# Kernel optimization log

Hardware: AMD Instinct MI355X
Metric: run time of the kernel (lower is better)

Reference implementation:

```python
import jax, jax.numpy as jnp
import numpy as np

N_NODES = 100000
N_EDGES = 3200000
NFEAT = 512
HDIM = 64
NCLASS = 40
N_LAYERS = 4
NEG_SLOPE = 0.2


def setup_inputs() -> dict:
    key = jax.random.key(0)
    ks = jax.random.split(key, 10)
    x = jax.random.normal(ks[0], (N_NODES, NFEAT), dtype=jnp.float32)
    edge_index = jax.random.randint(ks[1], (2, N_EDGES), 0, N_NODES, dtype=jnp.int64)
    s = 0.1
    return {
        "x": x,
        "edge_index": edge_index,
        "W_in": jax.random.normal(ks[2], (NFEAT, HDIM), dtype=jnp.float32) * s,
        "b_in": jnp.zeros((HDIM,), dtype=jnp.float32),
        "W_conv": jax.random.normal(ks[3], (N_LAYERS, HDIM, HDIM), dtype=jnp.float32) * s,
        "att_src": jax.random.normal(ks[4], (N_LAYERS, HDIM), dtype=jnp.float32) * s,
        "att_dst": jax.random.normal(ks[5], (N_LAYERS, HDIM), dtype=jnp.float32) * s,
        "b_conv": jnp.zeros((N_LAYERS, HDIM), dtype=jnp.float32),
        "W_out": jax.random.normal(ks[6], (HDIM, NCLASS), dtype=jnp.float32) * s,
        "b_out": jnp.zeros((NCLASS,), dtype=jnp.float32),
    }


def _gat_conv(x, src, dst, W, a_src_w, a_dst_w, bias):
    # PyG GATConv, heads=1, concat=True, add_self_loops handled by caller.
    N = x.shape[0]
    h = x @ W  # [N, H]
    a_src = h @ a_src_w  # [N]
    a_dst = h @ a_dst_w  # [N]
    e = jax.nn.leaky_relu(a_src[src] + a_dst[dst], NEG_SLOPE)  # [E]
    # segment softmax over edges grouped by destination node
    m = jax.ops.segment_max(e, dst, num_segments=N)
    ex = jnp.exp(e - m[dst])
    denom = jax.ops.segment_sum(ex, dst, num_segments=N)
    alpha = ex / denom[dst]
    out = jax.ops.segment_sum(alpha[:, None] * h[src], dst, num_segments=N)
    return out + bias


def reference(x, edge_index, W_in, b_in, W_conv, att_src, att_dst, b_conv, W_out, b_out):
    N = x.shape[0]
    # add self-loops (PyG GATConv default)
    loop = jnp.arange(N, dtype=edge_index.dtype)
    src = jnp.concatenate([edge_index[0], loop])
    dst = jnp.concatenate([edge_index[1], loop])

    h = x @ W_in + b_in  # lnin
    for l in range(N_LAYERS):
        h_in = h
        h = jax.nn.elu(_gat_conv(h, src, dst, W_conv[l], att_src[l], att_dst[l], b_conv[l]))
        h = h_in + h  # residual
    return h @ W_out + b_out  # lnout
```

## Files before the change

kernel.cpp:

```cpp
#include <hip/hip_runtime.h>
#include <hip/hip_bf16.h>
#include <hip/hip_fp16.h>

#define N_NODES 100000
#define N_EDGES 3200000
#define NFEAT 512
#define HDIM 64
#define NCLASS 40
#define N_LAYERS 4
#define NEG_SLOPE 0.2f

#define BATCH 4096
#define PBLOCKS ((N_EDGES + BATCH - 1) / BATCH)
#define SCUR_PAD 16

#define NB2 ((N_NODES + 255) / 256)
#define CAP2 9216
#define NCOUNT (NB2 * SCUR_PAD)

typedef __attribute__((ext_vector_type(8))) _Float16 half8;
typedef __attribute__((ext_vector_type(4))) float floatx4;

__device__ __forceinline__ float leaky(float x) {
    return x >= 0.f ? x : NEG_SLOPE * x;
}

__global__ void zero_counters_kernel(int* __restrict__ p) {
    int i = blockIdx.x * blockDim.x + threadIdx.x;
    if (i < NCOUNT) p[i] = 0;
}


__global__ __launch_bounds__(256) void partition_direct_kernel(const int* __restrict__ ei,
                                                               int* __restrict__ scur2,
                                                               unsigned* __restrict__ pairs2) {
    __shared__ unsigned buf[BATCH];
    __shared__ int cnt[NB2];
    __shared__ int off[NB2 + 1];
    __shared__ int gb[NB2];
    int t = threadIdx.x;
    long long base = (long long)blockIdx.x * BATCH;

    unsigned key[16];
    int bn[16];
    for (int i = t; i < NB2; i += 256) cnt[i] = 0;
    __syncthreads();

#pragma unroll
    for (int i = 0; i < 16; ++i) {
        long long e = base + i * 256 + t;
        if (e < N_EDGES) {
            int s = ei[e];
            int d = ei[N_EDGES + e];
            int b = d >> 8;
            bn[i] = b;
            key[i] = (unsigned)s | ((unsigned)(d & 255) << 17);
            atomicAdd(&cnt[b], 1);
        } else {
            bn[i] = -1;
        }
    }
    __syncthreads();
    if (t == 0) {
        int run = 0;
        for (int s2 = 0; s2 < NB2; ++s2) { off[s2] = run; run += cnt[s2]; }
        off[NB2] = run;
    }
    __syncthreads();
    for (int i = t; i < NB2; i += 256) {
        int c = cnt[i];
        gb[i] = c ? atomicAdd(&scur2[i * SCUR_PAD], c) : 0;
        cnt[i] = 0;
    }
    __syncthreads();
#pragma unroll
    for (int i = 0; i < 16; ++i) {
        if (bn[i] >= 0) {
            int p = atomicAdd(&cnt[bn[i]], 1);
            buf[off[bn[i]] + p] = key[i];
        }
    }
    __syncthreads();
    int total = off[NB2];
    for (int p = t; p < total; p += 256) {
        int lo = 0, hi = NB2 - 1;
        while (lo < hi) {
            int mid = (lo + hi + 1) >> 1;
            if (off[mid] <= p) lo = mid; else hi = mid - 1;
        }
        int idx = gb[lo] + (p - off[lo]);
        if (idx < CAP2) pairs2[(size_t)lo * CAP2 + idx] = buf[p];
    }
}

__global__ __launch_bounds__(512) void scan_buckets_kernel(const int* __restrict__ scur2,
                                                           int* __restrict__ bbase) {
    __shared__ int s[512];
    int t = threadIdx.x;
    int v = 0;
    if (t < NB2) {
        v = scur2[t * SCUR_PAD];
        if (v > CAP2) v = CAP2;
    }
    s[t] = v;
    __syncthreads();
    for (int off = 1; off < 512; off <<= 1) {
        int x = (t >= off) ? s[t - off] : 0;
        __syncthreads();
        s[t] += x;
        __syncthreads();
    }
    if (t < NB2) bbase[t] = s[t] - v;
    if (t == NB2 - 1) bbase[NB2] = s[t];
}

__global__ __launch_bounds__(256) void bucket_sort_kernel(const int* __restrict__ scur2,
                                                          const int* __restrict__ bbase,
                                                          const unsigned* __restrict__ pairs2,
                                                          int* __restrict__ col,
                                                          int* __restrict__ rp) {
    __shared__ int hist[256];
    __shared__ int cur[256];
    __shared__ unsigned outb[CAP2];
    int b = blockIdx.x;
    int c = scur2[b * SCUR_PAD]; if (c > CAP2) c = CAP2;
    const unsigned* seg = pairs2 + (size_t)b * CAP2;
    int t = threadIdx.x;
    int nlo = b * 256;
    int nnodes = N_NODES - nlo; if (nnodes > 256) nnodes = 256;
    hist[t] = 0;
    __syncthreads();
    for (int i = t; i < c; i += 256) atomicAdd(&hist[(seg[i] >> 17) & 255], 1);
    __syncthreads();
    int v = hist[t];
    for (int off = 1; off < 256; off <<= 1) {
        int x = (t >= off) ? hist[t - off] : 0;
        __syncthreads();
        hist[t] += x;
        __syncthreads();
    }
    int excl = hist[t] - v;
    cur[t] = excl;
    int base = bbase[b];
    if (t < nnodes) rp[nlo + t] = base + excl;
    if (b == NB2 - 1 && t == 0) rp[N_NODES] = base + c;
    __syncthreads();
    for (int i = t; i < c; i += 256) {
        unsigned k = seg[i];
        int p = atomicAdd(&cur[(k >> 17) & 255], 1);
        outb[p] = k & 0x1FFFFu;
    }
    __syncthreads();
    for (int i = t; i < c; i += 256) col[base + i] = (int)outb[i];
}


__global__ __launch_bounds__(256) void gemm_in_mfma(const float* __restrict__ A,
                                                    const float* __restrict__ B,
                                                    const float* __restrict__ bias,
                                                    float* __restrict__ C, int M) {
    __shared__ _Float16 As[2][64][40];
    __shared__ _Float16 Bt[2][64][40];
    int t = threadIdx.x;
    int lane = t & 63;
    int wid = t >> 6;
    int row0 = blockIdx.x * 64;

    floatx4 acc[4];
#pragma unroll
    for (int ct = 0; ct < 4; ++ct) acc[ct] = (floatx4){0.f, 0.f, 0.f, 0.f};

#define STAGE_A(buf, kt)                                                           \
    {                                                                              \
        int r = t >> 2, kq = (t & 3) << 3;                                         \
        int gr = row0 + r;                                                         \
        float4 v0 = make_float4(0.f, 0.f, 0.f, 0.f), v1 = v0;                      \
        if (gr < M) {                                                              \
            v0 = *(const float4*)&A[(size_t)gr * 512 + (kt) * 32 + kq];            \
            v1 = *(const float4*)&A[(size_t)gr * 512 + (kt) * 32 + kq + 4];        \
        }                                                                          \
        half8 h;                                                                   \
        h[0] = (_Float16)v0.x; h[1] = (_Float16)v0.y;                              \
        h[2] = (_Float16)v0.z; h[3] = (_Float16)v0.w;                              \
        h[4] = (_Float16)v1.x; h[5] = (_Float16)v1.y;                              \
        h[6] = (_Float16)v1.z; h[7] = (_Float16)v1.w;                              \
        *(half8*)&As[buf][r][kq] = h;                                              \
    }

#define STAGE_B(buf, kt)                                                           \
    {                                                                              \
        int k = t >> 3, n0 = (t & 7) << 3;                                         \
        float4 w0 = *(const float4*)&B[(size_t)((kt) * 32 + k) * 64 + n0];         \
        float4 w1 = *(const float4*)&B[(size_t)((kt) * 32 + k) * 64 + n0 + 4];     \
        Bt[buf][n0 + 0][k] = (_Float16)w0.x; Bt[buf][n0 + 1][k] = (_Float16)w0.y;  \
        Bt[buf][n0 + 2][k] = (_Float16)w0.z; Bt[buf][n0 + 3][k] = (_Float16)w0.w;  \
        Bt[buf][n0 + 4][k] = (_Float16)w1.x; Bt[buf][n0 + 5][k] = (_Float16)w1.y;  \
        Bt[buf][n0 + 6][k] = (_Float16)w1.z; Bt[buf][n0 + 7][k] = (_Float16)w1.w;  \
    }

    STAGE_A(0, 0)
    STAGE_B(0, 0)
    __syncthreads();
    for (int kt = 0; kt < 16; ++kt) {
        int buf = kt & 1;
        if (kt < 15) {
            STAGE_A(buf ^ 1, kt + 1)
            STAGE_B(buf ^ 1, kt + 1)
        }
        half8 a = *(half8*)&As[buf][wid * 16 + (lane & 15)][(lane >> 4) * 8];
#pragma unroll
        for (int ct = 0; ct < 4; ++ct) {
            half8 b = *(half8*)&Bt[buf][ct * 16 + (lane & 15)][(lane >> 4) * 8];
            acc[ct] = __builtin_amdgcn_mfma_f32_16x16x32_f16(a, b, acc[ct], 0, 0, 0);
        }
        __syncthreads();
    }
#pragma unroll
    for (int ct = 0; ct < 4; ++ct) {
        int colg = ct * 16 + (lane & 15);
        float bv = bias[colg];
#pragma unroll
        for (int i = 0; i < 4; ++i) {
            int gr = row0 + wid * 16 + (lane >> 4) * 4 + i;
            if (gr < M) C[(size_t)gr * 64 + colg] = acc[ct][i] + bv;
        }
    }
#undef STAGE_A
#undef STAGE_B
}


__global__ __launch_bounds__(256) void gemm_fused_mfma(const float* __restrict__ A,
                                                       const float* __restrict__ W,
                                                       const float* __restrict__ att_s_g,
                                                       const float* __restrict__ att_d_g,
                                                       float* __restrict__ as_,
                                                       float* __restrict__ ad_,
                                                       __half* __restrict__ h2h, int M) {
    __shared__ _Float16 As[64][72];
    __shared__ _Float16 Wt[64][72];
    __shared__ float sATT[128];
    int t = threadIdx.x;
    int lane = t & 63;
    int wid = t >> 6;
    int row0 = blockIdx.x * 64;
    if (t < 128) sATT[t] = (t < 64) ? att_s_g[t] : att_d_g[t - 64];

    {
        int r = t >> 2, kq = (t & 3) << 4;
        int gr = row0 + r;
        float4 v0 = make_float4(0.f, 0.f, 0.f, 0.f), v1 = v0, v2 = v0, v3 = v0;
        if (gr < M) {
            const float* ap = &A[(size_t)gr * 64 + kq];
            v0 = *(const float4*)(ap + 0);
            v1 = *(const float4*)(ap + 4);
            v2 = *(const float4*)(ap + 8);
            v3 = *(const float4*)(ap + 12);
        }
        half8 h0, h1;
        h0[0] = (_Float16)v0.x; h0[1] = (_Float16)v0.y; h0[2] = (_Float16)v0.z; h0[3] = (_Float16)v0.w;
        h0[4] = (_Float16)v1.x; h0[5] = (_Float16)v1.y; h0[6] = (_Float16)v1.z; h0[7] = (_Float16)v1.w;
        h1[0] = (_Float16)v2.x; h1[1] = (_Float16)v2.y; h1[2] = (_Float16)v2.z; h1[3] = (_Float16)v2.w;
        h1[4] = (_Float16)v3.x; h1[5] = (_Float16)v3.y; h1[6] = (_Float16)v3.z; h1[7] = (_Float16)v3.w;
        *(half8*)&As[r][kq] = h0;
        *(half8*)&As[r][kq + 8] = h1;
    }
    {
        int k = t >> 2, n0 = (t & 3) << 4;
        const float* wp = &W[(size_t)k * 64 + n0];
        float4 w0 = *(const float4*)(wp + 0);
        float4 w1 = *(const float4*)(wp + 4);
        float4 w2 = *(const float4*)(wp + 8);
        float4 w3 = *(const float4*)(wp + 12);
        float wv[16] = {w0.x, w0.y, w0.z, w0.w, w1.x, w1.y, w1.z, w1.w,
                        w2.x, w2.y, w2.z, w2.w, w3.x, w3.y, w3.z, w3.w};
#pragma unroll
        for (int j = 0; j < 16; ++j) Wt[n0 + j][k] = (_Float16)wv[j];
    }
    __syncthreads();

    floatx4 acc[4];
#pragma unroll
    for (int ct = 0; ct < 4; ++ct) acc[ct] = (floatx4){0.f, 0.f, 0.f, 0.f};
#pragma unroll
    for (int kt = 0; kt < 2; ++kt) {
        half8 a = *(half8*)&As[wid * 16 + (lane & 15)][kt * 32 + (lane >> 4) * 8];
#pragma unroll
        for (int ct = 0; ct < 4; ++ct) {
            half8 b = *(half8*)&Wt[ct * 16 + (lane & 15)][kt * 32 + (lane >> 4) * 8];
            acc[ct] = __builtin_amdgcn_mfma_f32_16x16x32_f16(a, b, acc[ct], 0, 0, 0);
        }
    }

    int c15 = lane & 15;
    float ps[4] = {0.f, 0.f, 0.f, 0.f}, pd[4] = {0.f, 0.f, 0.f, 0.f};
#pragma unroll
    for (int ct = 0; ct < 4; ++ct) {
        float sa = sATT[ct * 16 + c15];
        float sd = sATT[64 + ct * 16 + c15];
#pragma unroll
        for (int i = 0; i < 4; ++i) {
            ps[i] += acc[ct][i] * sa;
            pd[i] += acc[ct][i] * sd;
        }
    }
#pragma unroll
    for (int off = 1; off < 16; off <<= 1) {
#pragma unroll
        for (int i = 0; i < 4; ++i) {
            ps[i] += __shfl_xor(ps[i], off);
            pd[i] += __shfl_xor(pd[i], off);
        }
    }
    if (c15 == 0) {
#pragma unroll
        for (int i = 0; i < 4; ++i) {
            int gr = row0 + wid * 16 + (lane >> 4) * 4 + i;
            if (gr < M) { as_[gr] = ps[i]; ad_[gr] = pd[i]; }
        }
    }
#pragma unroll
    for (int ct = 0; ct < 4; ++ct) {
        int colg = ct * 16 + c15;
#pragma unroll
        for (int i = 0; i < 4; ++i) {
            int gr = row0 + wid * 16 + (lane >> 4) * 4 + i;
            if (gr < M) h2h[(size_t)gr * 64 + colg] = __float2half(acc[ct][i]);
        }
    }
}


__global__ __launch_bounds__(256) void gat_aggregate(const int* __restrict__ rp,
                                                     const int* __restrict__ col,
                                                     const __half* __restrict__ h2h,
                                                     const float* __restrict__ as_,
                                                     const float* __restrict__ ad_,
                                                     const float* __restrict__ bias,
                                                     float* __restrict__ h ) {
    __shared__ int2 sw[4][64];
    int wv = threadIdx.x >> 6;
    int wid = blockIdx.x * 4 + wv;
    int lane = threadIdx.x & 63;
    if (wid >= N_NODES) return;
    int beg = rp[wid];
    int end = rp[wid + 1];
    float adv = ad_[wid];
    float m = leaky(as_[wid] + adv);

    float acc = __half2float(h2h[(size_t)wid * 64 + lane]);
    float wsum = 0.f;

    for (int j0 = beg; j0 < end; j0 += 64) {
        int rem = end - j0;
        int cnt = rem < 64 ? rem : 64;
        if (lane < cnt) {
            int s = col[j0 + lane];
            float w = __expf(leaky(as_[s] + adv) - m);
            wsum += w;
            sw[wv][lane] = make_int2(s, __float_as_int(w));
        }
        int j = 0;
        for (; j + 8 <= cnt; j += 8) {
            int2 p[8];
#pragma unroll
            for (int q = 0; q < 8; ++q) p[q] = sw[wv][j + q];
            __half hv[8];
#pragma unroll
            for (int q = 0; q < 8; ++q) hv[q] = h2h[(size_t)p[q].x * 64 + lane];
#pragma unroll
            for (int q = 0; q < 8; ++q)
                acc = fmaf(__int_as_float(p[q].y), __half2float(hv[q]), acc);
        }
        for (; j < cnt; ++j) {
            int2 p = sw[wv][j];
            acc = fmaf(__int_as_float(p.y),
                       __half2float(h2h[(size_t)p.x * 64 + lane]), acc);
        }
    }
#pragma unroll
    for (int off = 32; off; off >>= 1) wsum += __shfl_xor(wsum, off);
    float denom = wsum + 1.0f;

    float o = acc / denom + bias[lane];
    float e = (o > 0.f) ? o : expm1f(o);
    size_t idx = (size_t)wid * 64 + lane;
    h[idx] = h[idx] + e;
}


__global__ __launch_bounds__(256) void out_gemm(const float* __restrict__ h,
                                                const float* __restrict__ W,
                                                const float* __restrict__ b,
                                                float* __restrict__ out) {
    __shared__ float Ws[64 * 40];
    __shared__ float bs[40];
    int t = threadIdx.x;
    for (int idx = t; idx < 64 * 40; idx += 256) Ws[idx] = W[idx];
    if (t < 40) bs[t] = b[t];
    __syncthreads();
    int wid = blockIdx.x * (blockDim.x >> 6) + (t >> 6);
    int lane = t & 63;
    if (wid >= N_NODES) return;
    float hv = h[(size_t)wid * 64 + lane];
    float acc = (lane < 40) ? bs[lane] : 0.f;
#pragma unroll
    for (int k = 0; k < 64; ++k) {
        float hk = __shfl(hv, k);
        float wv = (lane < 40) ? Ws[k * 40 + lane] : 0.f;
        acc += hk * wv;
    }
    if (lane < 40) out[(size_t)wid * 40 + lane] = acc;
}


extern "C" void kernel_launch(void* const* d_in, const int* in_sizes, int n_in,
                              void* d_out, int out_size, void* d_ws, size_t ws_size,
                              hipStream_t stream) {
    const float* x        = (const float*)d_in[0];
    const int* ei         = (const int*)d_in[1];
    const float* W_in     = (const float*)d_in[2];
    const float* b_in     = (const float*)d_in[3];
    const float* W_conv   = (const float*)d_in[4];
    const float* att_src  = (const float*)d_in[5];
    const float* att_dst  = (const float*)d_in[6];
    const float* b_conv   = (const float*)d_in[7];
    const float* W_out    = (const float*)d_in[8];
    const float* b_out    = (const float*)d_in[9];
    float* out = (float*)d_out;

    char* w = (char*)d_ws;
    float*    hA    = (float*)w;    w += (size_t)N_NODES * 64 * 4;
    __half*   h2h   = (__half*)w;   w += (size_t)N_NODES * 64 * 2;
    float*    as_   = (float*)w;    w += (size_t)N_NODES * 4;
    float*    ad_   = (float*)w;    w += (size_t)N_NODES * 4;
    int*      rp    = (int*)w;      w += 400016;
    int*      scur2 = (int*)w;      w += NB2 * SCUR_PAD * 4;
    int*      bbase = (int*)w;      w += 4096;
    int*      col   = (int*)w;      w += (size_t)N_EDGES * 4;
    unsigned* pairs2= (unsigned*)w; w += (size_t)NB2 * CAP2 * 4;

    zero_counters_kernel<<<(NCOUNT + 255) / 256, 256, 0, stream>>>(scur2);
    partition_direct_kernel<<<PBLOCKS, 256, 0, stream>>>(ei, scur2, pairs2);
    scan_buckets_kernel<<<1, 512, 0, stream>>>(scur2, bbase);
    bucket_sort_kernel<<<NB2, 256, 0, stream>>>(scur2, bbase, pairs2, col, rp);

    gemm_in_mfma<<<(N_NODES + 63) / 64, 256, 0, stream>>>(x, W_in, b_in, hA, N_NODES);

    for (int l = 0; l < N_LAYERS; ++l) {
        gemm_fused_mfma<<<(N_NODES + 63) / 64, 256, 0, stream>>>(hA, W_conv + (size_t)l * 64 * 64,
                                                                 att_src + l * 64, att_dst + l * 64,
                                                                 as_, ad_, h2h, N_NODES);
        gat_aggregate<<<N_NODES / 4, 256, 0, stream>>>(rp, col, h2h, as_, ad_,
                                                       b_conv + l * 64, hA);
    }

    out_gemm<<<N_NODES / 4, 256, 0, stream>>>(hA, W_out, b_out, out);
}
```

Measured before the change: 611.9 us.

## Process two nodes per wavefront in aggregation and fuse output GEMM into last layer

The GAT aggregation kernel now handles two consecutive destination nodes per wavefront, packing both nodes' edge lists into shared 64-edge chunks and routing each contribution to a per-node accumulator. This targets the underused lanes and wasted iterations when a node's degree is not a multiple of 64. A templated variant for the final layer also computes the 64x40 output projection in-kernel from shared memory, removing the separate out_gemm launch and the final write and re-read of h. The cost is per-edge branching between the two accumulators and extra shared-memory use, which may lower occupancy in the fused variant.

```diff
diff --git a/kernel.cpp b/kernel.cpp
--- a/kernel.cpp
+++ b/kernel.cpp
@@ -331,33 +331,53 @@
 }
 
 
-__global__ __launch_bounds__(256) void gat_aggregate(const int* __restrict__ rp,
-                                                     const int* __restrict__ col,
-                                                     const __half* __restrict__ h2h,
-                                                     const float* __restrict__ as_,
-                                                     const float* __restrict__ ad_,
-                                                     const float* __restrict__ bias,
-                                                     float* __restrict__ h ) {
+template <bool FUSE_OUT>
+__global__ __launch_bounds__(256) void gat_aggregate_t(const int* __restrict__ rp,
+                                                       const int* __restrict__ col,
+                                                       const __half* __restrict__ h2h,
+                                                       const float* __restrict__ as_,
+                                                       const float* __restrict__ ad_,
+                                                       const float* __restrict__ bias,
+                                                       float* __restrict__ h,
+                                                       const float* __restrict__ W_out,
+                                                       const float* __restrict__ b_out,
+                                                       float* __restrict__ out) {
     __shared__ int2 sw[4][64];
-    int wv = threadIdx.x >> 6;
-    int wid = blockIdx.x * 4 + wv;
-    int lane = threadIdx.x & 63;
-    if (wid >= N_NODES) return;
-    int beg = rp[wid];
-    int end = rp[wid + 1];
-    float adv = ad_[wid];
-    float m = leaky(as_[wid] + adv);
-
-    float acc = __half2float(h2h[(size_t)wid * 64 + lane]);
-    float wsum = 0.f;
+    __shared__ float sh[4][64];
+    __shared__ float Ws[64 * 40];
+    __shared__ float bs[40];
+    int t = threadIdx.x;
+    int wv = t >> 6;
+    int lane = t & 63;
+    if (FUSE_OUT) {
+        for (int i = t; i < 64 * 40; i += 256) Ws[i] = W_out[i];
+        if (t < 40) bs[t] = b_out[t];
+        __syncthreads();
+    }
+    int n0 = (blockIdx.x * 4 + wv) * 2;
+
+    int beg = rp[n0];
+    int mid = rp[n0 + 1];
+    int end = rp[n0 + 2];
+    float adv0 = ad_[n0], adv1 = ad_[n0 + 1];
+    float m0 = leaky(as_[n0] + adv0);
+    float m1 = leaky(as_[n0 + 1] + adv1);
+
+    float acc0 = __half2float(h2h[(size_t)n0 * 64 + lane]);
+    float acc1 = __half2float(h2h[(size_t)(n0 + 1) * 64 + lane]);
+    float wsum0 = 0.f, wsum1 = 0.f;
 
     for (int j0 = beg; j0 < end; j0 += 64) {
         int rem = end - j0;
         int cnt = rem < 64 ? rem : 64;
         if (lane < cnt) {
-            int s = col[j0 + lane];
+            int j = j0 + lane;
+            int s = col[j];
+            bool is1 = (j >= mid);
+            float adv = is1 ? adv1 : adv0;
+            float m = is1 ? m1 : m0;
             float w = __expf(leaky(as_[s] + adv) - m);
-            wsum += w;
+            if (is1) wsum1 += w; else wsum0 += w;
             sw[wv][lane] = make_int2(s, __float_as_int(w));
         }
         int j = 0;
@@ -369,48 +389,53 @@
 #pragma unroll
             for (int q = 0; q < 8; ++q) hv[q] = h2h[(size_t)p[q].x * 64 + lane];
 #pragma unroll
-            for (int q = 0; q < 8; ++q)
-                acc = fmaf(__int_as_float(p[q].y), __half2float(hv[q]), acc);
+            for (int q = 0; q < 8; ++q) {
+                float w = __int_as_float(p[q].y);
+                float v = __half2float(hv[q]);
+                if (j0 + j + q < mid) acc0 = fmaf(w, v, acc0);
+                else                  acc1 = fmaf(w, v, acc1);
+            }
         }
         for (; j < cnt; ++j) {
             int2 p = sw[wv][j];
-            acc = fmaf(__int_as_float(p.y),
-                       __half2float(h2h[(size_t)p.x * 64 + lane]), acc);
-        }
-    }
-#pragma unroll
-    for (int off = 32; off; off >>= 1) wsum += __shfl_xor(wsum, off);
-    float denom = wsum + 1.0f;
-
-    float o = acc / denom + bias[lane];
-    float e = (o > 0.f) ? o : expm1f(o);
-    size_t idx = (size_t)wid * 64 + lane;
-    h[idx] = h[idx] + e;
-}
-
-
-__global__ __launch_bounds__(256) void out_gemm(const float* __restrict__ h,
-                                                const float* __restrict__ W,
-                                                const float* __restrict__ b,
-                                                float* __restrict__ out) {
-    __shared__ float Ws[64 * 40];
-    __shared__ float bs[40];
-    int t = threadIdx.x;
-    for (int idx = t; idx < 64 * 40; idx += 256) Ws[idx] = W[idx];
-    if (t < 40) bs[t] = b[t];
-    __syncthreads();
-    int wid = blockIdx.x * (blockDim.x >> 6) + (t >> 6);
-    int lane = t & 63;
-    if (wid >= N_NODES) return;
-    float hv = h[(size_t)wid * 64 + lane];
-    float acc = (lane < 40) ? bs[lane] : 0.f;
-#pragma unroll
-    for (int k = 0; k < 64; ++k) {
-        float hk = __shfl(hv, k);
-        float wv = (lane < 40) ? Ws[k * 40 + lane] : 0.f;
-        acc += hk * wv;
-    }
-    if (lane < 40) out[(size_t)wid * 40 + lane] = acc;
+            float w = __int_as_float(p.y);
+            float v = __half2float(h2h[(size_t)p.x * 64 + lane]);
+            if (j0 + j < mid) acc0 = fmaf(w, v, acc0);
+            else              acc1 = fmaf(w, v, acc1);
+        }
+    }
+#pragma unroll
+    for (int off = 32; off; off >>= 1) {
+        wsum0 += __shfl_xor(wsum0, off);
+        wsum1 += __shfl_xor(wsum1, off);
+    }
+    float bv = bias[lane];
+    float o0 = acc0 / (wsum0 + 1.0f) + bv;
+    float o1 = acc1 / (wsum1 + 1.0f) + bv;
+    float e0 = (o0 > 0.f) ? o0 : expm1f(o0);
+    float e1 = (o1 > 0.f) ? o1 : expm1f(o1);
+    float h0 = h[(size_t)n0 * 64 + lane] + e0;
+    float h1 = h[(size_t)(n0 + 1) * 64 + lane] + e1;
+
+    if constexpr (!FUSE_OUT) {
+        h[(size_t)n0 * 64 + lane] = h0;
+        h[(size_t)(n0 + 1) * 64 + lane] = h1;
+    } else {
+        sw[wv][lane] = make_int2(0, 0);
+        sh[wv][lane] = h0;
+        float o = (lane < 40) ? bs[lane] : 0.f;
+#pragma unroll 8
+        for (int k = 0; k < 64; ++k)
+            o = fmaf(sh[wv][k], (lane < 40) ? Ws[k * 40 + lane] : 0.f, o);
+        if (lane < 40) out[(size_t)n0 * 40 + lane] = o;
+
+        sh[wv][lane] = h1;
+        float o2 = (lane < 40) ? bs[lane] : 0.f;
+#pragma unroll 8
+        for (int k = 0; k < 64; ++k)
+            o2 = fmaf(sh[wv][k], (lane < 40) ? Ws[k * 40 + lane] : 0.f, o2);
+        if (lane < 40) out[(size_t)(n0 + 1) * 40 + lane] = o2;
+    }
 }
 
 
@@ -447,13 +472,19 @@
 
     gemm_in_mfma<<<(N_NODES + 63) / 64, 256, 0, stream>>>(x, W_in, b_in, hA, N_NODES);
 
+    int agg_blocks = N_NODES / 8;
     for (int l = 0; l < N_LAYERS; ++l) {
         gemm_fused_mfma<<<(N_NODES + 63) / 64, 256, 0, stream>>>(hA, W_conv + (size_t)l * 64 * 64,
                                                                  att_src + l * 64, att_dst + l * 64,
                                                                  as_, ad_, h2h, N_NODES);
-        gat_aggregate<<<N_NODES / 4, 256, 0, stream>>>(rp, col, h2h, as_, ad_,
-                                                       b_conv + l * 64, hA);
-    }
-
-    out_gemm<<<N_NODES / 4, 256, 0, stream>>>(hA, W_out, b_out, out);
-}
+        if (l < N_LAYERS - 1) {
+            gat_aggregate_t<false><<<agg_blocks, 256, 0, stream>>>(rp, col, h2h, as_, ad_,
+                                                                   b_conv + l * 64, hA,
+                                                                   nullptr, nullptr, nullptr);
+        } else {
+            gat_aggregate_t<true><<<agg_blocks, 256, 0, stream>>>(rp, col, h2h, as_, ad_,
+                                                                  b_conv + l * 64, hA,
+                                                                  W_out, b_out, out);
+        }
+    }
+}
```

Result: faster. 523.0 us (-14.5%).
